# Optimization experiments

Measured on AMD Instinct MI355X. Metric: run time of the kernel, lower is better.

The kernel has to match this reference:

```python
import math
import jax, jax.numpy as jnp
import numpy as np

B, N, D, H, R = 2, 2048, 1024, 16, 32
DK = D // H


def _alibi_bias(n_heads, n_tokens):
    # faithful port of _alibi_slopes + alibi_bias (n_heads, n_tokens are static ints)
    def pow2slopes(n):
        start = 2.0 ** (-(2.0 ** (-(math.log2(n) - 3))))
        return [start * (start ** i) for i in range(n)]
    if math.log2(n_heads).is_integer():
        vals = pow2slopes(n_heads)
    else:
        closest = 2 ** math.floor(math.log2(n_heads))
        vals = pow2slopes(closest) + pow2slopes(2 * closest)[0::2][: n_heads - closest]
    slopes = jnp.asarray(vals, dtype=jnp.float32).reshape(1, n_heads, 1, 1)
    i = jnp.arange(n_tokens).reshape(1, 1, n_tokens, 1)
    j = jnp.arange(n_tokens).reshape(1, 1, 1, n_tokens)
    dist = jnp.maximum(j - i, 0).astype(jnp.float32)
    return -slopes * dist  # [1, h, n, n]


def setup_inputs() -> dict:
    key = jax.random.key(0)
    ks = jax.random.split(key, 6)
    x = jax.random.normal(ks[0], (B, N, D), dtype=jnp.float32)
    s = 0.02
    Wq = jax.random.normal(ks[1], (D, D), dtype=jnp.float32) * s
    Wk = jax.random.normal(ks[2], (D, D), dtype=jnp.float32) * s
    Wv = jax.random.normal(ks[3], (D, D), dtype=jnp.float32) * s
    Wproj = jax.random.normal(ks[4], (D, D), dtype=jnp.float32) * s
    # orthogonal init of U [dk, r] via QR (orthonormal columns)
    U, _ = jnp.linalg.qr(jax.random.normal(ks[5], (DK, R), dtype=jnp.float32))
    # additive causal mask (0 on/below diagonal, -1e9 above)
    i = jnp.arange(N).reshape(N, 1)
    j = jnp.arange(N).reshape(1, N)
    mask = jnp.where(j <= i, 0.0, -1e9).astype(jnp.float32).reshape(1, 1, N, N)
    return {"x": x, "Wq": Wq, "Wk": Wk, "Wv": Wv, "U": U, "Wproj": Wproj,
            "mask": mask, "h": H, "rel_bias_tokens": N}


def reference(x, Wq, Wk, Wv, U, Wproj, mask, h, rel_bias_tokens):
    b, n, d = x.shape
    dk = d // h
    scale = 1.0 / math.sqrt(dk)  # note: scaled by sqrt(dk), not sqrt(r)

    def proj_qk(y):  # [b,n,d] -> [b,h,n,r]
        return jnp.einsum('bnhk,kr->bhnr', y.reshape(b, n, h, dk), U)

    q = proj_qk(x @ Wq.T)
    k = proj_qk(x @ Wk.T)
    v = (x @ Wv.T).reshape(b, n, h, dk).transpose(0, 2, 1, 3)  # [b,h,n,dk]

    att = jnp.einsum('bhqr,bhkr->bhqk', q, k) * scale  # [b,h,n,n]
    bias = _alibi_bias(h, rel_bias_tokens)[:, :, -n:, :]
    att = att + bias + mask
    z = jnp.einsum('bhqk,bhkd->bhqd', jax.nn.softmax(att, axis=-1), v)
    z = z.transpose(0, 2, 1, 3).reshape(b, n, h * dk)
    out = z @ Wproj.T  # dropout is identity in eval
    return out
```

## Files before the change

kernel.cpp:

```cpp
#include <hip/hip_runtime.h>
#include <math.h>

#define B_   2
#define N_   2048
#define D_   1024
#define H_   16
#define R_   32
#define DK_  64
#define HR_  512
#define QC_  2048
#define M_   4096

typedef __attribute__((ext_vector_type(8))) short  bf16x8;
typedef __attribute__((ext_vector_type(4))) float  f32x4;
typedef unsigned short ushort_t;

__device__ __forceinline__ unsigned short bf16_rne(float f) {
    unsigned u = __float_as_uint(f);
    unsigned r = (u + 0x7FFFu + ((u >> 16) & 1u)) >> 16;
    return (unsigned short)r;
}
__device__ __forceinline__ float bf16_to_f(unsigned short h) {
    return __uint_as_float(((unsigned)h) << 16);
}
__device__ __forceinline__ void gload_lds16(const void* g, void* l) {
    __builtin_amdgcn_global_load_lds(
        (const __attribute__((address_space(1))) unsigned int*)g,
        (__attribute__((address_space(3))) unsigned int*)l, 16, 0, 0);
}

__global__ __launch_bounds__(256) void build_bmat2(
    const float* __restrict__ Wq, const float* __restrict__ Wk,
    const float* __restrict__ Wv, const float* __restrict__ U,
    ushort_t* __restrict__ BhT, ushort_t* __restrict__ BlT)
{
    int idx = blockIdx.x * 256 + threadIdx.x;
    int e = idx >> 10;
    int d = idx & 1023;
    float val;
    if (e < 1024) {
        const float* W = (e < 512) ? Wq : Wk;
        int eh = e & 511;
        int h = eh >> 5;
        int r = eh & 31;
        float acc = 0.f;
        #pragma unroll
        for (int kk = 0; kk < DK_; ++kk)
            acc = fmaf(W[(size_t)(h*DK_ + kk)*D_ + d], U[kk*R_ + r], acc);
        val = (e < 512) ? acc * 0.125f : acc;
    } else {
        val = Wv[(size_t)(e - 1024)*D_ + d];
    }
    unsigned short h16 = bf16_rne(val);
    BhT[idx] = h16;
    BlT[idx] = bf16_rne(val - bf16_to_f(h16));
}

__global__ __launch_bounds__(256) void cvt_hl(
    const float* __restrict__ src, ushort_t* __restrict__ dh,
    ushort_t* __restrict__ dl)
{
    int i = blockIdx.x * 256 + threadIdx.x;
    float4 v = ((const float4*)src)[i];
    unsigned short h0 = bf16_rne(v.x), h1 = bf16_rne(v.y),
                   h2 = bf16_rne(v.z), h3 = bf16_rne(v.w);
    ((ushort4*)dh)[i] = make_ushort4(h0, h1, h2, h3);
    ((ushort4*)dl)[i] = make_ushort4(bf16_rne(v.x - bf16_to_f(h0)),
                                     bf16_rne(v.y - bf16_to_f(h1)),
                                     bf16_rne(v.z - bf16_to_f(h2)),
                                     bf16_rne(v.w - bf16_to_f(h3)));
}

template<int EPI>
__global__ __launch_bounds__(256) void gemm_hl(
    const ushort_t* __restrict__ Ah, const ushort_t* __restrict__ Al,
    const ushort_t* __restrict__ Bh, const ushort_t* __restrict__ Bl,
    float* __restrict__ C,
    ushort_t* __restrict__ Qh, ushort_t* __restrict__ Ql,
    ushort_t* __restrict__ Kh, ushort_t* __restrict__ Kl,
    float* __restrict__ Vf,
    int M, int Nn, int K)
{
    __shared__ __attribute__((aligned(16))) ushort_t lds[4][128][32];
    int nb = Nn >> 7;
    int bx = blockIdx.x % nb, by = blockIdx.x / nb;
    int m0 = by << 7, n0 = bx << 7;
    int tid = threadIdx.x;
    int wave = tid >> 6, lane = tid & 63;
    int wr = wave >> 1, wc = wave & 1;

    const ushort_t* gsrc = (wave == 0) ? Ah : (wave == 1) ? Al
                         : (wave == 2) ? Bh : Bl;
    int row0 = (wave < 2) ? m0 : n0;
    int rloc  = lane >> 2;
    int kslot = lane & 3;

    f32x4 acc[4][4];
    #pragma unroll
    for (int i = 0; i < 4; ++i)
        #pragma unroll
        for (int j = 0; j < 4; ++j)
            acc[i][j] = (f32x4){0.f, 0.f, 0.f, 0.f};

    char* ldsb = (char*)&lds[0][0][0];

    for (int k0 = 0; k0 < K; k0 += 32) {
        #pragma unroll
        for (int seg = 0; seg < 8; ++seg) {
            int r = seg*16 + rloc;
            int ksw = (kslot << 4) ^ (((r >> 1) & 3) << 4);
            const ushort_t* gp = gsrc + (size_t)(row0 + r)*K + k0 + (ksw >> 1);
            gload_lds16(gp, ldsb + wave*8192 + seg*1024);
        }
        asm volatile("s_waitcnt vmcnt(0)" ::: "memory");
        __syncthreads();

        bf16x8 a_h[4], a_l[4];
        #pragma unroll
        for (int mf = 0; mf < 4; ++mf) {
            int r  = wr*64 + mf*16 + (lane & 15);
            int kb = ((lane >> 4) << 4) ^ (((r >> 1) & 3) << 4);
            a_h[mf] = *(const bf16x8*)(ldsb +        r*64 + kb);
            a_l[mf] = *(const bf16x8*)(ldsb + 8192 + r*64 + kb);
        }
        #pragma unroll
        for (int nf = 0; nf < 4; ++nf) {
            int r  = wc*64 + nf*16 + (lane & 15);
            int kb = ((lane >> 4) << 4) ^ (((r >> 1) & 3) << 4);
            bf16x8 b_h = *(const bf16x8*)(ldsb + 16384 + r*64 + kb);
            bf16x8 b_l = *(const bf16x8*)(ldsb + 24576 + r*64 + kb);
            #pragma unroll
            for (int mf = 0; mf < 4; ++mf)
                acc[mf][nf] = __builtin_amdgcn_mfma_f32_16x16x32_bf16(
                    a_h[mf], b_h, acc[mf][nf], 0, 0, 0);
            #pragma unroll
            for (int mf = 0; mf < 4; ++mf)
                acc[mf][nf] = __builtin_amdgcn_mfma_f32_16x16x32_bf16(
                    a_h[mf], b_l, acc[mf][nf], 0, 0, 0);
            #pragma unroll
            for (int mf = 0; mf < 4; ++mf)
                acc[mf][nf] = __builtin_amdgcn_mfma_f32_16x16x32_bf16(
                    a_l[mf], b_h, acc[mf][nf], 0, 0, 0);
        }
        __syncthreads();
    }
    int cr = (lane >> 4) << 2;
    int cc = lane & 15;
    #pragma unroll
    for (int mf = 0; mf < 4; ++mf)
        #pragma unroll
        for (int nf = 0; nf < 4; ++nf) {
            int rr = m0 + wr*64 + mf*16 + cr;
            int c  = n0 + wc*64 + nf*16 + cc;
            #pragma unroll
            for (int rg = 0; rg < 4; ++rg) {
                float v = acc[mf][nf][rg];
                if (EPI == 0) {
                    C[(size_t)(rr + rg)*Nn + c] = v;
                } else {
                    int t = rr + rg;
                    if (n0 < 512) {
                        unsigned short h16 = bf16_rne(v);
                        Qh[(size_t)t*HR_ + c] = h16;
                        Ql[(size_t)t*HR_ + c] = bf16_rne(v - bf16_to_f(h16));
                    } else if (n0 < 1024) {
                        unsigned short h16 = bf16_rne(v);
                        Kh[(size_t)t*HR_ + c - 512] = h16;
                        Kl[(size_t)t*HR_ + c - 512] = bf16_rne(v - bf16_to_f(h16));
                    } else {
                        Vf[(size_t)t*D_ + c - 1024] = v;
                    }
                }
            }
        }
}

__global__ __launch_bounds__(256) void cvtVT(
    const float* __restrict__ Vf, ushort_t* __restrict__ VTh,
    ushort_t* __restrict__ VTl)
{
    __shared__ float Ls[64][65];
    int blk = blockIdx.x;
    int bh = blk >> 5, kvt = blk & 31;
    int b = bh >> 4, hh = bh & 15;
    int tid = threadIdx.x;
    int t0 = b*N_ + kvt*64;
    int u = tid >> 4, v = tid & 15;
    #pragma unroll
    for (int p = 0; p < 4; ++p) {
        int r = p*16 + u;
        int c4 = v*4;
        float4 x4 = *(const float4*)(Vf + (size_t)(t0 + r)*D_ + hh*64 + c4);
        Ls[r][c4+0] = x4.x; Ls[r][c4+1] = x4.y;
        Ls[r][c4+2] = x4.z; Ls[r][c4+3] = x4.w;
    }
    __syncthreads();
    #pragma unroll
    for (int p = 0; p < 4; ++p) {
        int d = p*16 + u;
        int kvb = v*4;
        float f0 = Ls[kvb+0][d], f1 = Ls[kvb+1][d],
              f2 = Ls[kvb+2][d], f3 = Ls[kvb+3][d];
        unsigned short h0 = bf16_rne(f0), h1 = bf16_rne(f1),
                       h2 = bf16_rne(f2), h3 = bf16_rne(f3);
        size_t o = ((size_t)(bh*64 + d))*N_ + kvt*64 + kvb;
        *(ushort4*)(VTh + o) = make_ushort4(h0, h1, h2, h3);
        *(ushort4*)(VTl + o) = make_ushort4(bf16_rne(f0 - bf16_to_f(h0)),
                                            bf16_rne(f1 - bf16_to_f(h1)),
                                            bf16_rne(f2 - bf16_to_f(h2)),
                                            bf16_rne(f3 - bf16_to_f(h3)));
    }
}

__device__ __forceinline__ void attn_tile(
    int kvt, int qt, int qb, int bN, int bh, int c, int g,
    const bf16x8 (&kh)[2], const bf16x8 (&kl)[2],
    const bf16x8 (&qh)[2], const bf16x8 (&ql)[2],
    const ushort_t* __restrict__ VTh, const ushort_t* __restrict__ VTl,
    f32x4 (&acc)[2][4], float (&lsum)[2])
{
    const float MCONST = 12.0f;
    int kv0 = kvt*32;
    bf16x8 vh[4], vl[4];
    #pragma unroll
    for (int ds = 0; ds < 4; ++ds) {
        size_t vo = ((size_t)(bh*64 + ds*16 + c))*N_ + kv0 + g*8;
        vh[ds] = *(const bf16x8*)(VTh + vo);
        vl[ds] = *(const bf16x8*)(VTl + vo);
    }
    f32x4 s[2][2];
    #pragma unroll
    for (int qs = 0; qs < 2; ++qs)
        #pragma unroll
        for (int ks = 0; ks < 2; ++ks) {
            f32x4 t = (f32x4){0.f, 0.f, 0.f, 0.f};
            t = __builtin_amdgcn_mfma_f32_16x16x32_bf16(kh[ks], qh[qs], t, 0, 0, 0);
            t = __builtin_amdgcn_mfma_f32_16x16x32_bf16(kl[ks], qh[qs], t, 0, 0, 0);
            t = __builtin_amdgcn_mfma_f32_16x16x32_bf16(kh[ks], ql[qs], t, 0, 0, 0);
            s[qs][ks] = t;
        }
    bool needmask = (kvt == qt);
    bf16x8 pH[2], pL[2];
    #pragma unroll
    for (int qs = 0; qs < 2; ++qs) {
        int q = qb + qs*16 + c;
        float p[8];
        #pragma unroll
        for (int ks = 0; ks < 2; ++ks)
            #pragma unroll
            for (int r = 0; r < 4; ++r) {
                float sv = s[qs][ks][r];
                if (needmask && (kv0 + 8*g + ks*4 + r > q)) sv = -1e30f;
                p[ks*4 + r] = __expf(sv - MCONST);
            }
        lsum[qs] += ((p[0]+p[1]) + (p[2]+p[3])) + ((p[4]+p[5]) + (p[6]+p[7]));
        #pragma unroll
        for (int j = 0; j < 8; ++j) {
            unsigned pb = __float_as_uint(p[j]);
            pH[qs][j] = (short)(pb >> 16);
            float hi = __uint_as_float(pb & 0xFFFF0000u);
            pL[qs][j] = (short)(__float_as_uint(p[j] - hi) >> 16);
        }
    }
    #pragma unroll
    for (int ds = 0; ds < 4; ++ds)
        #pragma unroll
        for (int qs = 0; qs < 2; ++qs) {
            acc[qs][ds] = __builtin_amdgcn_mfma_f32_16x16x32_bf16(
                vh[ds], pH[qs], acc[qs][ds], 0, 0, 0);
            acc[qs][ds] = __builtin_amdgcn_mfma_f32_16x16x32_bf16(
                vh[ds], pL[qs], acc[qs][ds], 0, 0, 0);
            acc[qs][ds] = __builtin_amdgcn_mfma_f32_16x16x32_bf16(
                vl[ds], pH[qs], acc[qs][ds], 0, 0, 0);
        }
}

__global__ __launch_bounds__(256) void attn6(
    const ushort_t* __restrict__ Qbh, const ushort_t* __restrict__ Qbl,
    const ushort_t* __restrict__ Kbh, const ushort_t* __restrict__ Kbl,
    const ushort_t* __restrict__ VTh, const ushort_t* __restrict__ VTl,
    ushort_t* __restrict__ zh, ushort_t* __restrict__ zl)
{
    __shared__ float mg[3][64][36];
    __shared__ float ots[16][68];
    int bIdx = blockIdx.x;
    int pr = bIdx >> 5;
    int bh = bIdx & 31;
    int b = bh >> 4, hh = bh & 15;
    int tid = threadIdx.x;
    int wave = tid >> 6, lane = tid & 63;
    int c = lane & 15, g = lane >> 4;
    int kpa = 8*(c >> 2) + (c & 3);
    int bN = b*N_;

    #pragma unroll 1
    for (int hf = 0; hf < 2; ++hf) {
        int qt = hf ? pr : 63 - pr;
        int qb = qt << 5;
        int nkt = qt + 1;

        bf16x8 qh[2], ql[2];
        #pragma unroll
        for (int qs = 0; qs < 2; ++qs) {
            size_t qo = ((size_t)(bN + qb + qs*16 + c))*HR_ + hh*R_ + g*8;
            qh[qs] = *(const bf16x8*)(Qbh + qo);
            ql[qs] = *(const bf16x8*)(Qbl + qo);
        }
        f32x4 acc[2][4];
        #pragma unroll
        for (int qs = 0; qs < 2; ++qs)
            #pragma unroll
            for (int ds = 0; ds < 4; ++ds)
                acc[qs][ds] = (f32x4){0.f, 0.f, 0.f, 0.f};
        float lsum[2] = {0.f, 0.f};

        #define LOADK(KVT, KH, KL)                                            \
            _Pragma("unroll")                                                 \
            for (int ks = 0; ks < 2; ++ks) {                                  \
                size_t ko = ((size_t)(bN + (KVT)*32 + kpa + ks*4))*HR_        \
                            + hh*R_ + g*8;                                    \
                KH[ks] = *(const bf16x8*)(Kbh + ko);                          \
                KL[ks] = *(const bf16x8*)(Kbl + ko);                          \
            }

        bf16x8 khA[2], klA[2], khB[2], klB[2];
        int kvt = wave;
        if (kvt < nkt) {
            LOADK(kvt, khA, klA);
            while (true) {
                int kv2 = kvt + 4;
                if (kv2 < nkt) { LOADK(kv2, khB, klB); }
                attn_tile(kvt, qt, qb, bN, bh, c, g, khA, klA, qh, ql,
                          VTh, VTl, acc, lsum);
                if (kv2 >= nkt) break;
                int kv3 = kv2 + 4;
                if (kv3 < nkt) { LOADK(kv3, khA, klA); }
                attn_tile(kv2, qt, qb, bN, bh, c, g, khB, klB, qh, ql,
                          VTh, VTl, acc, lsum);
                if (kv3 >= nkt) break;
                kvt = kv3;
            }
        }
        #undef LOADK

        #pragma unroll
        for (int qs = 0; qs < 2; ++qs) {
            lsum[qs] += __shfl_xor(lsum[qs], 16);
            lsum[qs] += __shfl_xor(lsum[qs], 32);
        }

        if (wave != 0) {
            int w = wave - 1;
            #pragma unroll
            for (int qs = 0; qs < 2; ++qs)
                #pragma unroll
                for (int ds = 0; ds < 4; ++ds)
                    *(float4*)(&mg[w][lane][qs*16 + ds*4]) =
                        make_float4(acc[qs][ds][0], acc[qs][ds][1],
                                    acc[qs][ds][2], acc[qs][ds][3]);
            mg[w][lane][32] = lsum[0];
            mg[w][lane][33] = lsum[1];
        }
        __syncthreads();
        if (wave == 0) {
            #pragma unroll
            for (int qs = 0; qs < 2; ++qs) {
                float lt = lsum[qs] + mg[0][lane][32 + qs]
                         + mg[1][lane][32 + qs] + mg[2][lane][32 + qs];
                float inv = 1.0f / lt;
                #pragma unroll
                for (int ds = 0; ds < 4; ++ds)
                    #pragma unroll
                    for (int rg = 0; rg < 4; ++rg)
                        acc[qs][ds][rg] = (acc[qs][ds][rg]
                            + mg[0][lane][qs*16 + ds*4 + rg]
                            + mg[1][lane][qs*16 + ds*4 + rg]
                            + mg[2][lane][qs*16 + ds*4 + rg]) * inv;
            }
            #pragma unroll
            for (int qs = 0; qs < 2; ++qs) {
                #pragma unroll
                for (int ds = 0; ds < 4; ++ds)
                    #pragma unroll
                    for (int rg = 0; rg < 4; ++rg)
                        ots[c][ds*16 + g*4 + rg] = acc[qs][ds][rg];
                int qr = lane >> 2;
                size_t trow = (size_t)(bN + qb + qs*16 + qr);
                #pragma unroll
                for (int j4 = 0; j4 < 4; ++j4) {
                    int d0 = j4*16 + (lane & 3)*4;
                    float4 v4 = *(const float4*)(&ots[qr][d0]);
                    unsigned short h0 = bf16_rne(v4.x), h1 = bf16_rne(v4.y),
                                   h2 = bf16_rne(v4.z), h3 = bf16_rne(v4.w);
                    *(ushort4*)(zh + trow*D_ + hh*64 + d0) =
                        make_ushort4(h0, h1, h2, h3);
                    *(ushort4*)(zl + trow*D_ + hh*64 + d0) =
                        make_ushort4(bf16_rne(v4.x - bf16_to_f(h0)),
                                     bf16_rne(v4.y - bf16_to_f(h1)),
                                     bf16_rne(v4.z - bf16_to_f(h2)),
                                     bf16_rne(v4.w - bf16_to_f(h3)));
                }
            }
        }
        __syncthreads();
    }
}

extern "C" void kernel_launch(void* const* d_in, const int* in_sizes, int n_in,
                              void* d_out, int out_size, void* d_ws, size_t ws_size,
                              hipStream_t stream)
{
    (void)in_sizes; (void)n_in; (void)out_size; (void)ws_size;
    const float* x  = (const float*)d_in[0];
    const float* Wq = (const float*)d_in[1];
    const float* Wk = (const float*)d_in[2];
    const float* Wv = (const float*)d_in[3];
    const float* U  = (const float*)d_in[4];
    const float* Wp = (const float*)d_in[5];
    float* out = (float*)d_out;

    const size_t MB = 1048576;
    char* w = (char*)d_ws;
    float*    Vf  = (float*)   (w);
    ushort_t* Qbh = (ushort_t*)(w + 16*MB);
    ushort_t* Qbl = (ushort_t*)(w + 20*MB);
    ushort_t* Kbh = (ushort_t*)(w + 24*MB);
    ushort_t* Kbl = (ushort_t*)(w + 28*MB);
    ushort_t* BhT = (ushort_t*)(w + 32*MB);
    ushort_t* BlT = (ushort_t*)(w + 36*MB);
    ushort_t* wph = (ushort_t*)(w + 40*MB);
    ushort_t* wpl = (ushort_t*)(w + 42*MB);
    ushort_t* xzh = (ushort_t*)(w + 44*MB);
    ushort_t* xzl = (ushort_t*)(w + 52*MB);
    ushort_t* VTh = (ushort_t*)(w + 44*MB);
    ushort_t* VTl = (ushort_t*)(w + 52*MB);
    ushort_t* zh  = (ushort_t*)(w);
    ushort_t* zl  = (ushort_t*)(w + 8*MB);

    build_bmat2<<<dim3(8192), dim3(256), 0, stream>>>(Wq, Wk, Wv, U, BhT, BlT);
    cvt_hl<<<dim3(4096), dim3(256), 0, stream>>>(x, xzh, xzl);
    cvt_hl<<<dim3(1024), dim3(256), 0, stream>>>(Wp, wph, wpl);
    gemm_hl<1><<<dim3(512), dim3(256), 0, stream>>>(
        xzh, xzl, BhT, BlT, nullptr, Qbh, Qbl, Kbh, Kbl, Vf, M_, QC_, D_);
    cvtVT<<<dim3(1024), dim3(256), 0, stream>>>(Vf, VTh, VTl);
    attn6<<<dim3(1024), dim3(256), 0, stream>>>(
        Qbh, Qbl, Kbh, Kbl, VTh, VTl, zh, zl);
    gemm_hl<0><<<dim3(256), dim3(256), 0, stream>>>(
        zh, zl, wph, wpl, out, nullptr, nullptr, nullptr, nullptr, nullptr,
        M_, D_, D_);
}
```

Measured before the change: 326.3 us.

## Pre-pack Q, K and V into MFMA fragment order for contiguous attention loads

The projection GEMM epilogue and the V transpose kernel now write Q, K and V hi/lo bf16 splits directly in the per-lane MFMA fragment order the attention kernel consumes. Each wave can then load its 16-byte fragments as one fully contiguous 1KB chunk per wave instead of strided row gathers. The cost is scattered 2-byte stores in the GEMM epilogue and more index arithmetic there.

```diff
diff --git a/kernel.cpp b/kernel.cpp
--- a/kernel.cpp
+++ b/kernel.cpp
@@ -76,8 +76,8 @@
     const ushort_t* __restrict__ Ah, const ushort_t* __restrict__ Al,
     const ushort_t* __restrict__ Bh, const ushort_t* __restrict__ Bl,
     float* __restrict__ C,
-    ushort_t* __restrict__ Qh, ushort_t* __restrict__ Ql,
-    ushort_t* __restrict__ Kh, ushort_t* __restrict__ Kl,
+    ushort_t* __restrict__ Qph, ushort_t* __restrict__ Qpl,
+    ushort_t* __restrict__ Kph, ushort_t* __restrict__ Kpl,
     float* __restrict__ Vf,
     int M, int Nn, int K)
 {
@@ -159,14 +159,26 @@
                     C[(size_t)(rr + rg)*Nn + c] = v;
                 } else {
                     int t = rr + rg;
+                    int bb = t >> 11, n = t & 2047;
+                    unsigned short h16 = bf16_rne(v);
+                    unsigned short l16 = bf16_rne(v - bf16_to_f(h16));
                     if (n0 < 512) {
-                        unsigned short h16 = bf16_rne(v);
-                        Qh[(size_t)t*HR_ + c] = h16;
-                        Ql[(size_t)t*HR_ + c] = bf16_rne(v - bf16_to_f(h16));
+                        int hh = c >> 5, r = c & 31;
+                        int qt = n >> 5, qs = (n >> 4) & 1, cq = n & 15;
+                        int g = r >> 3, j = r & 7;
+                        size_t o = ((((size_t)(bb*16 + hh)*64 + qt)*2 + qs)*64
+                                    + g*16 + cq)*8 + j;
+                        Qph[o] = h16;  Qpl[o] = l16;
                     } else if (n0 < 1024) {
-                        unsigned short h16 = bf16_rne(v);
-                        Kh[(size_t)t*HR_ + c - 512] = h16;
-                        Kl[(size_t)t*HR_ + c - 512] = bf16_rne(v - bf16_to_f(h16));
+                        int ck = c - 512;
+                        int hh = ck >> 5, r = ck & 31;
+                        int kvt = n >> 5, kr = n & 31;
+                        int c4 = ((kr >> 3) << 2) | (kr & 3);
+                        int ks = (kr >> 2) & 1;
+                        int g = r >> 3, j = r & 7;
+                        size_t o = ((((size_t)(bb*16 + hh)*64 + kvt)*2 + ks)*64
+                                    + g*16 + c4)*8 + j;
+                        Kph[o] = h16;  Kpl[o] = l16;
                     } else {
                         Vf[(size_t)t*D_ + c - 1024] = v;
                     }
@@ -175,16 +187,16 @@
         }
 }
 
-__global__ __launch_bounds__(256) void cvtVT(
-    const float* __restrict__ Vf, ushort_t* __restrict__ VTh,
-    ushort_t* __restrict__ VTl)
+__global__ __launch_bounds__(256) void cvtVTp(
+    const float* __restrict__ Vf, ushort_t* __restrict__ Vph,
+    ushort_t* __restrict__ Vpl)
 {
     __shared__ float Ls[64][65];
     int blk = blockIdx.x;
-    int bh = blk >> 5, kvt = blk & 31;
+    int bh = blk >> 5, kvt64 = blk & 31;
     int b = bh >> 4, hh = bh & 15;
     int tid = threadIdx.x;
-    int t0 = b*N_ + kvt*64;
+    int t0 = b*N_ + kvt64*64;
     int u = tid >> 4, v = tid & 15;
     #pragma unroll
     for (int p = 0; p < 4; ++p) {
@@ -203,9 +215,13 @@
               f2 = Ls[kvb+2][d], f3 = Ls[kvb+3][d];
         unsigned short h0 = bf16_rne(f0), h1 = bf16_rne(f1),
                        h2 = bf16_rne(f2), h3 = bf16_rne(f3);
-        size_t o = ((size_t)(bh*64 + d))*N_ + kvt*64 + kvb;
-        *(ushort4*)(VTh + o) = make_ushort4(h0, h1, h2, h3);
-        *(ushort4*)(VTl + o) = make_ushort4(bf16_rne(f0 - bf16_to_f(h0)),
+        int kvt = kvt64*2 + (kvb >> 5);
+        int kv5 = kvb & 31;
+        int g = kv5 >> 3, j0 = kv5 & 7;
+        int ds = d >> 4, cd = d & 15;
+        size_t o = ((((size_t)bh*64 + kvt)*4 + ds)*64 + g*16 + cd)*8 + j0;
+        *(ushort4*)(Vph + o) = make_ushort4(h0, h1, h2, h3);
+        *(ushort4*)(Vpl + o) = make_ushort4(bf16_rne(f0 - bf16_to_f(h0)),
                                             bf16_rne(f1 - bf16_to_f(h1)),
                                             bf16_rne(f2 - bf16_to_f(h2)),
                                             bf16_rne(f3 - bf16_to_f(h3)));
@@ -213,10 +229,10 @@
 }
 
 __device__ __forceinline__ void attn_tile(
-    int kvt, int qt, int qb, int bN, int bh, int c, int g,
+    int kvt, int qt, int qb, int bh, int c, int g, int lane,
     const bf16x8 (&kh)[2], const bf16x8 (&kl)[2],
     const bf16x8 (&qh)[2], const bf16x8 (&ql)[2],
-    const ushort_t* __restrict__ VTh, const ushort_t* __restrict__ VTl,
+    const ushort_t* __restrict__ Vph, const ushort_t* __restrict__ Vpl,
     f32x4 (&acc)[2][4], float (&lsum)[2])
 {
     const float MCONST = 12.0f;
@@ -224,9 +240,9 @@
     bf16x8 vh[4], vl[4];
     #pragma unroll
     for (int ds = 0; ds < 4; ++ds) {
-        size_t vo = ((size_t)(bh*64 + ds*16 + c))*N_ + kv0 + g*8;
-        vh[ds] = *(const bf16x8*)(VTh + vo);
-        vl[ds] = *(const bf16x8*)(VTl + vo);
+        size_t vo = ((((size_t)bh*64 + kvt)*4 + ds)*64 + lane)*8;
+        vh[ds] = *(const bf16x8*)(Vph + vo);
+        vl[ds] = *(const bf16x8*)(Vpl + vo);
     }
     f32x4 s[2][2];
     #pragma unroll
@@ -275,10 +291,10 @@
         }
 }
 
-__global__ __launch_bounds__(256) void attn6(
-    const ushort_t* __restrict__ Qbh, const ushort_t* __restrict__ Qbl,
-    const ushort_t* __restrict__ Kbh, const ushort_t* __restrict__ Kbl,
-    const ushort_t* __restrict__ VTh, const ushort_t* __restrict__ VTl,
+__global__ __launch_bounds__(256) void attn7(
+    const ushort_t* __restrict__ Qph, const ushort_t* __restrict__ Qpl,
+    const ushort_t* __restrict__ Kph, const ushort_t* __restrict__ Kpl,
+    const ushort_t* __restrict__ Vph, const ushort_t* __restrict__ Vpl,
     ushort_t* __restrict__ zh, ushort_t* __restrict__ zl)
 {
     __shared__ float mg[3][64][36];
@@ -290,7 +306,6 @@
     int tid = threadIdx.x;
     int wave = tid >> 6, lane = tid & 63;
     int c = lane & 15, g = lane >> 4;
-    int kpa = 8*(c >> 2) + (c & 3);
     int bN = b*N_;
 
     #pragma unroll 1
@@ -302,9 +317,9 @@
         bf16x8 qh[2], ql[2];
         #pragma unroll
         for (int qs = 0; qs < 2; ++qs) {
-            size_t qo = ((size_t)(bN + qb + qs*16 + c))*HR_ + hh*R_ + g*8;
-            qh[qs] = *(const bf16x8*)(Qbh + qo);
-            ql[qs] = *(const bf16x8*)(Qbl + qo);
+            size_t qo = ((((size_t)bh*64 + qt)*2 + qs)*64 + lane)*8;
+            qh[qs] = *(const bf16x8*)(Qph + qo);
+            ql[qs] = *(const bf16x8*)(Qpl + qo);
         }
         f32x4 acc[2][4];
         #pragma unroll
@@ -317,10 +332,9 @@
         #define LOADK(KVT, KH, KL)                                            \
             _Pragma("unroll")                                                 \
             for (int ks = 0; ks < 2; ++ks) {                                  \
-                size_t ko = ((size_t)(bN + (KVT)*32 + kpa + ks*4))*HR_        \
-                            + hh*R_ + g*8;                                    \
-                KH[ks] = *(const bf16x8*)(Kbh + ko);                          \
-                KL[ks] = *(const bf16x8*)(Kbl + ko);                          \
+                size_t ko = ((((size_t)bh*64 + (KVT))*2 + ks)*64 + lane)*8;   \
+                KH[ks] = *(const bf16x8*)(Kph + ko);                          \
+                KL[ks] = *(const bf16x8*)(Kpl + ko);                          \
             }
 
         bf16x8 khA[2], klA[2], khB[2], klB[2];
@@ -330,13 +344,13 @@
             while (true) {
                 int kv2 = kvt + 4;
                 if (kv2 < nkt) { LOADK(kv2, khB, klB); }
-                attn_tile(kvt, qt, qb, bN, bh, c, g, khA, klA, qh, ql,
-                          VTh, VTl, acc, lsum);
+                attn_tile(kvt, qt, qb, bh, c, g, lane, khA, klA, qh, ql,
+                          Vph, Vpl, acc, lsum);
                 if (kv2 >= nkt) break;
                 int kv3 = kv2 + 4;
                 if (kv3 < nkt) { LOADK(kv3, khA, klA); }
-                attn_tile(kv2, qt, qb, bN, bh, c, g, khB, klB, qh, ql,
-                          VTh, VTl, acc, lsum);
+                attn_tile(kv2, qt, qb, bh, c, g, lane, khB, klB, qh, ql,
+                          Vph, Vpl, acc, lsum);
                 if (kv3 >= nkt) break;
                 kvt = kv3;
             }
@@ -422,18 +436,18 @@
     const size_t MB = 1048576;
     char* w = (char*)d_ws;
     float*    Vf  = (float*)   (w);
-    ushort_t* Qbh = (ushort_t*)(w + 16*MB);
-    ushort_t* Qbl = (ushort_t*)(w + 20*MB);
-    ushort_t* Kbh = (ushort_t*)(w + 24*MB);
-    ushort_t* Kbl = (ushort_t*)(w + 28*MB);
+    ushort_t* Qph = (ushort_t*)(w + 16*MB);
+    ushort_t* Qpl = (ushort_t*)(w + 20*MB);
+    ushort_t* Kph = (ushort_t*)(w + 24*MB);
+    ushort_t* Kpl = (ushort_t*)(w + 28*MB);
     ushort_t* BhT = (ushort_t*)(w + 32*MB);
     ushort_t* BlT = (ushort_t*)(w + 36*MB);
     ushort_t* wph = (ushort_t*)(w + 40*MB);
     ushort_t* wpl = (ushort_t*)(w + 42*MB);
     ushort_t* xzh = (ushort_t*)(w + 44*MB);
     ushort_t* xzl = (ushort_t*)(w + 52*MB);
-    ushort_t* VTh = (ushort_t*)(w + 44*MB);
-    ushort_t* VTl = (ushort_t*)(w + 52*MB);
+    ushort_t* Vph = (ushort_t*)(w + 44*MB);
+    ushort_t* Vpl = (ushort_t*)(w + 52*MB);
     ushort_t* zh  = (ushort_t*)(w);
     ushort_t* zl  = (ushort_t*)(w + 8*MB);
 
@@ -441,10 +455,10 @@
     cvt_hl<<<dim3(4096), dim3(256), 0, stream>>>(x, xzh, xzl);
     cvt_hl<<<dim3(1024), dim3(256), 0, stream>>>(Wp, wph, wpl);
     gemm_hl<1><<<dim3(512), dim3(256), 0, stream>>>(
-        xzh, xzl, BhT, BlT, nullptr, Qbh, Qbl, Kbh, Kbl, Vf, M_, QC_, D_);
-    cvtVT<<<dim3(1024), dim3(256), 0, stream>>>(Vf, VTh, VTl);
-    attn6<<<dim3(1024), dim3(256), 0, stream>>>(
-        Qbh, Qbl, Kbh, Kbl, VTh, VTl, zh, zl);
+        xzh, xzl, BhT, BlT, nullptr, Qph, Qpl, Kph, Kpl, Vf, M_, QC_, D_);
+    cvtVTp<<<dim3(1024), dim3(256), 0, stream>>>(Vf, Vph, Vpl);
+    attn7<<<dim3(1024), dim3(256), 0, stream>>>(
+        Qph, Qpl, Kph, Kpl, Vph, Vpl, zh, zl);
     gemm_hl<0><<<dim3(256), dim3(256), 0, stream>>>(
         zh, zl, wph, wpl, out, nullptr, nullptr, nullptr, nullptr, nullptr,
         M_, D_, D_);
```

Result: faster. 283.6 us (-13.1%).
